# Optimization experiments

Hardware: AMD Instinct MI355X
Metric: run time of the kernel (lower is better)

The kernel has to match this reference:

```python
import jax, jax.numpy as jnp
import numpy as np

THETA = 10000.0


def apply_rope(t):
    """Partial rotary on first head_dim//2 dims, interleaved pairs (rotary_embedding_torch).
    t: (B, H, S, D) float32."""
    B, H, S, D = t.shape
    rot_dim = D // 2  # RotaryEmbedding(head_dim // 2)
    inv_freq = 1.0 / (THETA ** (jnp.arange(0, rot_dim, 2, dtype=jnp.float32) / rot_dim))  # (rot_dim//2,)
    pos = jnp.arange(S, dtype=jnp.float32)
    freqs = pos[:, None] * inv_freq[None, :]            # (S, rot_dim//2)
    freqs = jnp.repeat(freqs, 2, axis=-1)               # (S, rot_dim) interleaved
    cos, sin = jnp.cos(freqs), jnp.sin(freqs)           # (S, rot_dim)
    t_rot, t_pass = t[..., :rot_dim], t[..., rot_dim:]
    x1 = t_rot[..., 0::2]
    x2 = t_rot[..., 1::2]
    rot_half = jnp.stack((-x2, x1), axis=-1).reshape(t_rot.shape)
    t_rot = t_rot * cos + rot_half * sin
    return jnp.concatenate([t_rot, t_pass], axis=-1)


def setup_inputs() -> dict:
    key = jax.random.key(0)
    k1, k2, k3, k4, k5 = jax.random.split(key, 5)
    B, S, Dm = 2, 2048, 1024
    scale = 1.0 / np.sqrt(Dm)
    return {
        "x": jax.random.normal(k1, (B, S, Dm), dtype=jnp.float32),
        "Wqkv": jax.random.normal(k2, (3 * Dm, Dm), dtype=jnp.float32) * scale,
        "bqkv": jax.random.normal(k3, (3 * Dm,), dtype=jnp.float32) * 0.01,
        "Wout": jax.random.normal(k4, (Dm, Dm), dtype=jnp.float32) * scale,
        "bout": jax.random.normal(k5, (Dm,), dtype=jnp.float32) * 0.01,
    }


def reference(x, Wqkv, bqkv, Wout, bout):
    B, S, Dm = x.shape
    H = 16
    Dh = Dm // H
    qkv = x @ Wqkv.T + bqkv                              # (B, S, 3*Dm)
    qkv = qkv.reshape(B, S, 3, H, Dh).transpose(2, 0, 3, 1, 4)  # (3, B, H, S, Dh)
    q, k, v = qkv[0], qkv[1], qkv[2]
    q = apply_rope(q.astype(jnp.float32))
    k = apply_rope(k.astype(jnp.float32))
    scores = jnp.einsum("bhqd,bhkd->bhqk", q, k) / jnp.sqrt(jnp.float32(Dh))
    attn = jax.nn.softmax(scores, axis=-1)
    out = jnp.einsum("bhqk,bhkd->bhqd", attn, v)         # (B, H, S, Dh)
    out = out.transpose(0, 2, 1, 3).reshape(B, S, Dm)
    return out @ Wout.T + bout
```

## Files before the change

kernel.cpp:

```cpp
#include <hip/hip_runtime.h>

#define S_LEN 2048
#define DMODEL 1024
#define NHEAD 16
#define DHEAD 64
#define BATCH 2
#define BH_TOT (BATCH * NHEAD)
#define TOK (BATCH * S_LEN)
#define NQKV (3 * DMODEL)

#define QSCALE 0.18033688011112042f

typedef float  f32x4  __attribute__((ext_vector_type(4)));
typedef float  f32x16 __attribute__((ext_vector_type(16)));
typedef int    i32x4  __attribute__((ext_vector_type(4)));
typedef unsigned u32x2 __attribute__((ext_vector_type(2)));
typedef __bf16 bf16x8 __attribute__((ext_vector_type(8)));
typedef __bf16 bf16x4 __attribute__((ext_vector_type(4)));
typedef __bf16 bf16x2 __attribute__((ext_vector_type(2)));

typedef __attribute__((address_space(1))) void* as1_ptr;
typedef __attribute__((address_space(3))) void* as3_ptr;

__device__ __forceinline__ void gl2lds16(const void* g, void* l) {
  __builtin_amdgcn_global_load_lds((as1_ptr)(void*)g, (as3_ptr)l, 16, 0, 0);
}

__device__ __forceinline__ f32x4 mfma32(bf16x8 a, bf16x8 b, f32x4 c) {
  return __builtin_amdgcn_mfma_f32_16x16x32_bf16(a, b, c, 0, 0, 0);
}

__device__ __forceinline__ f32x16 mfma3216(bf16x8 a, bf16x8 b, f32x16 c) {
  return __builtin_amdgcn_mfma_f32_32x32x16_bf16(a, b, c, 0, 0, 0);
}

__device__ __forceinline__ unsigned pack2(float a, float b) {
  bf16x2 t;
  t[0] = (__bf16)a;
  t[1] = (__bf16)b;
  return __builtin_bit_cast(unsigned, t);
}

__device__ __forceinline__ bf16x8 pfragn(float a0, float a1, float a2, float a3,
                                         float a4, float a5, float a6, float a7) {
  const i32x4 w = {(int)pack2(a0, a1), (int)pack2(a2, a3),
                   (int)pack2(a4, a5), (int)pack2(a6, a7)};
  return __builtin_bit_cast(bf16x8, w);
}

__global__ __launch_bounds__(256) void cvt_kernel(const float* __restrict__ src,
                                                  __bf16* __restrict__ dst, int n) {
  const int i = (blockIdx.x * 256 + threadIdx.x) * 4;
  if (i >= n) return;
  const f32x4 v = *(const f32x4*)(src + i);
  bf16x4 o;
  o[0] = (__bf16)v[0]; o[1] = (__bf16)v[1]; o[2] = (__bf16)v[2]; o[3] = (__bf16)v[3];
  *(bf16x4*)(dst + i) = o;
}

__device__ __forceinline__ void gemm_tile_128(const __bf16* __restrict__ A,
                                              const __bf16* __restrict__ Bw,
                                              const int Kd, const int tileM, const int tileN,
                                              __bf16* As, __bf16* Bs, f32x4 acc[4][4]) {
  const int t    = threadIdx.x;
  const int lane = t & 63;
  const int wave = t >> 6;
  const int quad = lane >> 4;
  const int c    = lane & 15;
  const int wm   = (wave >> 1) << 6;
  const int wn   = (wave & 1) << 6;

  const int u0 = t, u1 = t + 256;
  const __bf16* gA0 = A  + (size_t)(tileM + (u0 >> 2)) * Kd + (u0 & 3) * 8;
  const __bf16* gA1 = A  + (size_t)(tileM + (u1 >> 2)) * Kd + (u1 & 3) * 8;
  const __bf16* gB0 = Bw + (size_t)(tileN + (u0 >> 2)) * Kd + (u0 & 3) * 8;
  const __bf16* gB1 = Bw + (size_t)(tileN + (u1 >> 2)) * Kd + (u1 & 3) * 8;
  __bf16* lA0 = As + u0 * 8; __bf16* lA1 = As + u1 * 8;
  __bf16* lB0 = Bs + u0 * 8; __bf16* lB1 = Bs + u1 * 8;

  for (int k0 = 0; k0 < Kd; k0 += 32) {
    gl2lds16(gA0 + k0, lA0);
    gl2lds16(gA1 + k0, lA1);
    gl2lds16(gB0 + k0, lB0);
    gl2lds16(gB1 + k0, lB1);
    __syncthreads();
    bf16x8 af[4], bfr[4];
#pragma unroll
    for (int mt = 0; mt < 4; ++mt)
      af[mt] = *(const bf16x8*)(As + (wm + mt * 16 + c) * 32 + quad * 8);
#pragma unroll
    for (int nt = 0; nt < 4; ++nt)
      bfr[nt] = *(const bf16x8*)(Bs + (wn + nt * 16 + c) * 32 + quad * 8);
#pragma unroll
    for (int mt = 0; mt < 4; ++mt)
#pragma unroll
      for (int nt = 0; nt < 4; ++nt)
        acc[mt][nt] = mfma32(af[mt], bfr[nt], acc[mt][nt]);
    __syncthreads();
  }
}

__global__ __launch_bounds__(256) void gemm_qkv_kernel(const __bf16* __restrict__ xb,
                                                       const __bf16* __restrict__ Wb,
                                                       const float* __restrict__ bias,
                                                       __bf16* __restrict__ Qb,
                                                       __bf16* __restrict__ Kb,
                                                       __bf16* __restrict__ Vtb) {
  __shared__ __align__(16) __bf16 As[128 * 32];
  __shared__ __align__(16) __bf16 Bs[128 * 32];
  f32x4 acc[4][4];
#pragma unroll
  for (int i = 0; i < 4; ++i)
#pragma unroll
    for (int j = 0; j < 4; ++j) acc[i][j] = (f32x4){0.f, 0.f, 0.f, 0.f};

  const int tileM = blockIdx.y * 128;
  const int tileN = blockIdx.x * 128;
  gemm_tile_128(xb, Wb, DMODEL, tileM, tileN, As, Bs, acc);

  const int t = threadIdx.x;
  const int lane = t & 63, wave = t >> 6;
  const int quad = lane >> 4, c = lane & 15;
  const int wm = (wave >> 1) << 6, wn = (wave & 1) << 6;

#pragma unroll
  for (int nt = 0; nt < 4; ++nt) {
    const int col = tileN + wn + nt * 16 + c;
    const float bv = bias[col];
    const int which = col >> 10;
    const int h  = (col >> 6) & 15;
    const int dh = col & 63;
    if (which == 2) {
#pragma unroll
      for (int mt = 0; mt < 4; ++mt) {
        const int row0 = tileM + wm + mt * 16 + quad * 4;
        const int bb = row0 >> 11;
        const int ss = row0 & (S_LEN - 1);
        bf16x4 o;
#pragma unroll
        for (int r = 0; r < 4; ++r) o[r] = (__bf16)(acc[mt][nt][r] + bv);
        *(bf16x4*)(Vtb + (((size_t)(bb * NHEAD + h)) * DHEAD + dh) * S_LEN + ss) = o;
      }
    } else {
      __bf16* dst = (which == 0) ? Qb : Kb;
      const float scl = (which == 0) ? QSCALE : 1.0f;
#pragma unroll
      for (int mt = 0; mt < 4; ++mt) {
#pragma unroll
        for (int r = 0; r < 4; ++r) {
          const int row = tileM + wm + mt * 16 + quad * 4 + r;
          const int bb = row >> 11;
          const int ss = row & (S_LEN - 1);
          dst[(((size_t)(bb * NHEAD + h)) * S_LEN + ss) * DHEAD + dh] =
              (__bf16)((acc[mt][nt][r] + bv) * scl);
        }
      }
    }
  }
}

__global__ __launch_bounds__(256) void gemm_out_kernel(const __bf16* __restrict__ AOb,
                                                       const __bf16* __restrict__ Wb,
                                                       const float* __restrict__ bout,
                                                       float* __restrict__ out) {
  __shared__ __align__(16) __bf16 As[128 * 32];
  __shared__ __align__(16) __bf16 Bs[128 * 32];
  f32x4 acc[4][4];
#pragma unroll
  for (int i = 0; i < 4; ++i)
#pragma unroll
    for (int j = 0; j < 4; ++j) acc[i][j] = (f32x4){0.f, 0.f, 0.f, 0.f};

  const int tileM = blockIdx.y * 128;
  const int tileN = blockIdx.x * 128;
  gemm_tile_128(AOb, Wb, DMODEL, tileM, tileN, As, Bs, acc);

  const int t = threadIdx.x;
  const int lane = t & 63, wave = t >> 6;
  const int quad = lane >> 4, c = lane & 15;
  const int wm = (wave >> 1) << 6, wn = (wave & 1) << 6;

#pragma unroll
  for (int nt = 0; nt < 4; ++nt) {
    const int col = tileN + wn + nt * 16 + c;
    const float bv = bout[col];
#pragma unroll
    for (int mt = 0; mt < 4; ++mt) {
#pragma unroll
      for (int r = 0; r < 4; ++r) {
        const int row = tileM + wm + mt * 16 + quad * 4 + r;
        out[(size_t)row * DMODEL + col] = acc[mt][nt][r] + bv;
      }
    }
  }
}

__global__ __launch_bounds__(256) void rope_kernel(__bf16* __restrict__ Qb, __bf16* __restrict__ Kb) {
  const int idx = blockIdx.x * 256 + threadIdx.x;
  const int j  = idx & 15;
  const int s  = (idx >> 4) & (S_LEN - 1);
  const int bh = (idx >> 15) & (BH_TOT - 1);
  __bf16* base = (idx >> 20) ? Kb : Qb;
  bf16x2* p = (bf16x2*)(base + ((size_t)bh * S_LEN + s) * DHEAD) + j;
  bf16x2 v = *p;
  const float x1 = (float)v[0];
  const float x2 = (float)v[1];
  const float LOG2_10000 = 13.287712379549449f;
  const float inv = exp2f(-(float)j * (LOG2_10000 / 16.0f));
  const float ang = (float)s * inv;
  float sn, cs;
  sincosf(ang, &sn, &cs);
  bf16x2 o;
  o[0] = (__bf16)(x1 * cs - x2 * sn);
  o[1] = (__bf16)(x2 * cs + x1 * sn);
  *p = o;
}

__global__ __launch_bounds__(64, 2) void attn_kernel(const __bf16* __restrict__ Qb,
                                                     const __bf16* __restrict__ Kb,
                                                     const __bf16* __restrict__ Vtb,
                                                     __bf16* __restrict__ AOb) {
  __shared__ __align__(16) __bf16 Ks[2][32 * 64];
  __shared__ __align__(16) __bf16 Vts[2][64 * 32];

  const int qt = blockIdx.x;
  const int bh = blockIdx.y;
  const int b = bh >> 4, h = bh & 15;
  const int lane = threadIdx.x & 63;
  const int c31 = lane & 31, hi = lane >> 5;
  const int cx7 = c31 & 7;
  const int cxv = (c31 >> 1) & 3;
  const size_t head = (size_t)bh * S_LEN * DHEAD;
  const int q0w = qt * 32;

  bf16x8 qf[4];
#pragma unroll
  for (int s = 0; s < 4; ++s)
    qf[s] = *(const bf16x8*)(Qb + head + (size_t)(q0w + c31) * DHEAD + s * 16 + hi * 8);

  f32x16 zzero;
#pragma unroll
  for (int i = 0; i < 16; ++i) zzero[i] = 0.f;

  f32x16 ota[2], otb[2];
  ota[0] = zzero; ota[1] = zzero; otb[0] = zzero; otb[1] = zzero;
  float lp = 0.f;

  const __bf16* kg[4];
  const __bf16* vg[4];
  int lofK[4], lofV[4];
#pragma unroll
  for (int i = 0; i < 4; ++i) {
    const int u = lane + 64 * i;
    const int rk = u >> 3, ck = (u & 7) ^ (rk & 7);
    kg[i] = Kb + head + (size_t)rk * DHEAD + ck * 8;
    lofK[i] = u * 8;
    const int rv = u >> 2, cv = (u & 3) ^ ((rv >> 1) & 3);
    vg[i] = Vtb + ((size_t)bh * DHEAD + rv) * S_LEN + cv * 8;
    lofV[i] = u * 8;
  }

#pragma unroll
  for (int i = 0; i < 4; ++i) {
    gl2lds16(kg[i], &Ks[0][lofK[i]]);
    gl2lds16(vg[i], &Vts[0][lofV[i]]);
  }

#define VFRAG(CUR, db, kc)                                                                 \
  __builtin_bit_cast(bf16x8, (i32x4){                                                      \
      (int)__builtin_bit_cast(u32x2, *(const bf16x4*)(&Vts[CUR][((db) * 32 + c31) * 32 +   \
                                     ((((kc) * 2) ^ cxv) * 8) + hi * 4]))[0],              \
      (int)__builtin_bit_cast(u32x2, *(const bf16x4*)(&Vts[CUR][((db) * 32 + c31) * 32 +   \
                                     ((((kc) * 2) ^ cxv) * 8) + hi * 4]))[1],              \
      (int)__builtin_bit_cast(u32x2, *(const bf16x4*)(&Vts[CUR][((db) * 32 + c31) * 32 +   \
                                     ((((kc) * 2 + 1) ^ cxv) * 8) + hi * 4]))[0],          \
      (int)__builtin_bit_cast(u32x2, *(const bf16x4*)(&Vts[CUR][((db) * 32 + c31) * 32 +   \
                                     ((((kc) * 2 + 1) ^ cxv) * 8) + hi * 4]))[1]})

#define ATTN_TILE(KB, CUR)                                                                 \
  {                                                                                        \
    asm volatile("s_waitcnt vmcnt(0)" ::: "memory");                                       \
    __builtin_amdgcn_sched_barrier(0);                                                     \
    bf16x8 kA[4];                                                                          \
    _Pragma("unroll")                                                                      \
    for (int s = 0; s < 4; ++s)                                                            \
      kA[s] = *(const bf16x8*)(&Ks[CUR][c31 * 64 + (((s * 2 + hi) ^ cx7) * 8)]);           \
    const bf16x8 vA00 = VFRAG(CUR, 0, 0);                                                  \
    const bf16x8 vA10 = VFRAG(CUR, 1, 0);                                                  \
    const bf16x8 vA01 = VFRAG(CUR, 0, 1);                                                  \
    const bf16x8 vA11 = VFRAG(CUR, 1, 1);                                                  \
    __builtin_amdgcn_sched_barrier(0);                                                     \
    if ((KB) + 1 < S_LEN / 32) {                                                           \
      const int ka = ((KB) + 1) * (32 * DHEAD);                                            \
      const int va = ((KB) + 1) * 32;                                                      \
      _Pragma("unroll")                                                                    \
      for (int i = 0; i < 4; ++i) {                                                        \
        gl2lds16(kg[i] + ka, &Ks[(CUR) ^ 1][lofK[i]]);                                     \
        gl2lds16(vg[i] + va, &Vts[(CUR) ^ 1][lofV[i]]);                                    \
      }                                                                                    \
    }                                                                                      \
    __builtin_amdgcn_sched_barrier(0);                                                     \
    f32x16 z = zzero;                                                                      \
    __builtin_amdgcn_s_setprio(1);                                                         \
    _Pragma("unroll")                                                                      \
    for (int s = 0; s < 4; ++s) z = mfma3216(kA[s], qf[s], z);                             \
    __builtin_amdgcn_s_setprio(0);                                                         \
    float p[16];                                                                           \
    _Pragma("unroll")                                                                      \
    for (int r = 0; r < 16; ++r) p[r] = __builtin_amdgcn_exp2f(z[r]);                      \
    lp += (((p[0] + p[1]) + (p[2] + p[3])) + ((p[4] + p[5]) + (p[6] + p[7])))              \
        + (((p[8] + p[9]) + (p[10] + p[11])) + ((p[12] + p[13]) + (p[14] + p[15])));       \
    const bf16x8 f0 = pfragn(p[0], p[1], p[2], p[3], p[4], p[5], p[6], p[7]);              \
    const bf16x8 f1 = pfragn(p[8], p[9], p[10], p[11], p[12], p[13], p[14], p[15]);        \
    __builtin_amdgcn_s_setprio(1);                                                         \
    ota[0] = mfma3216(vA00, f0, ota[0]);                                                   \
    ota[1] = mfma3216(vA10, f0, ota[1]);                                                   \
    otb[0] = mfma3216(vA01, f1, otb[0]);                                                   \
    otb[1] = mfma3216(vA11, f1, otb[1]);                                                   \
    __builtin_amdgcn_s_setprio(0);                                                         \
  }

  for (int kbb = 0; kbb < S_LEN / 64; ++kbb) {
    ATTN_TILE(2 * kbb, 0)
    ATTN_TILE(2 * kbb + 1, 1)
  }
#undef ATTN_TILE
#undef VFRAG

#pragma unroll
  for (int i = 0; i < 16; ++i) { ota[0][i] += otb[0][i]; ota[1][i] += otb[1][i]; }
  const float l = lp + __shfl_xor(lp, 32);
  const float inv = 1.0f / l;
  const int q = q0w + c31;
#pragma unroll
  for (int db = 0; db < 2; ++db) {
#pragma unroll
    for (int rg = 0; rg < 4; ++rg) {
      bf16x4 o;
#pragma unroll
      for (int i = 0; i < 4; ++i) o[i] = (__bf16)(ota[db][rg * 4 + i] * inv);
      const int d0 = db * 32 + rg * 8 + hi * 4;
      *(bf16x4*)(AOb + ((size_t)(b * S_LEN + q)) * DMODEL + h * DHEAD + d0) = o;
    }
  }
}

extern "C" void kernel_launch(void* const* d_in, const int* in_sizes, int n_in,
                              void* d_out, int out_size, void* d_ws, size_t ws_size,
                              hipStream_t stream) {
  const float* x    = (const float*)d_in[0];
  const float* Wqkv = (const float*)d_in[1];
  const float* bqkv = (const float*)d_in[2];
  const float* Wout = (const float*)d_in[3];
  const float* bout = (const float*)d_in[4];
  float* out = (float*)d_out;

  char* ws = (char*)d_ws;
  __bf16* xb    = (__bf16*)(ws + 0);
  __bf16* Wqkvb = (__bf16*)(ws + (size_t)8  * 1024 * 1024);
  __bf16* Woutb = (__bf16*)(ws + (size_t)14 * 1024 * 1024);
  __bf16* Qb    = (__bf16*)(ws + (size_t)16 * 1024 * 1024);
  __bf16* Kb    = (__bf16*)(ws + (size_t)24 * 1024 * 1024);
  __bf16* Vtb   = (__bf16*)(ws + (size_t)32 * 1024 * 1024);
  __bf16* AOb   = (__bf16*)(ws + (size_t)40 * 1024 * 1024);

  cvt_kernel<<<(TOK * DMODEL) / 1024, 256, 0, stream>>>(x, xb, TOK * DMODEL);
  cvt_kernel<<<(NQKV * DMODEL) / 1024, 256, 0, stream>>>(Wqkv, Wqkvb, NQKV * DMODEL);
  cvt_kernel<<<(DMODEL * DMODEL) / 1024, 256, 0, stream>>>(Wout, Woutb, DMODEL * DMODEL);

  gemm_qkv_kernel<<<dim3(NQKV / 128, TOK / 128), 256, 0, stream>>>(xb, Wqkvb, bqkv, Qb, Kb, Vtb);

  rope_kernel<<<(2 * BH_TOT * S_LEN * 16) / 256, 256, 0, stream>>>(Qb, Kb);

  attn_kernel<<<dim3(S_LEN / 32, BH_TOT), 64, 0, stream>>>(Qb, Kb, Vtb, AOb);

  gemm_out_kernel<<<dim3(DMODEL / 128, TOK / 128), 256, 0, stream>>>(AOb, Woutb, bout, out);
}
```

Baseline: 212.0 us.

## Share K/V tiles across two waves with 4-stage LDS prefetch pipeline

The attention kernel now runs two waves per block, each handling 32 query rows, so every K/V tile loaded into LDS serves 64 queries and global K/V traffic per query is halved. The LDS buffering grows from double to quad buffers with three tiles prefetched ahead, and waits use partial vmcnt counts instead of draining all loads. This adds a block barrier per tile and doubles LDS use per block, which may lower occupancy.

```diff
diff --git a/kernel.cpp b/kernel.cpp
--- a/kernel.cpp
+++ b/kernel.cpp
@@ -216,22 +216,23 @@
   *p = o;
 }
 
-__global__ __launch_bounds__(64, 2) void attn_kernel(const __bf16* __restrict__ Qb,
-                                                     const __bf16* __restrict__ Kb,
-                                                     const __bf16* __restrict__ Vtb,
-                                                     __bf16* __restrict__ AOb) {
-  __shared__ __align__(16) __bf16 Ks[2][32 * 64];
-  __shared__ __align__(16) __bf16 Vts[2][64 * 32];
+__global__ __launch_bounds__(128, 2) void attn_kernel(const __bf16* __restrict__ Qb,
+                                                      const __bf16* __restrict__ Kb,
+                                                      const __bf16* __restrict__ Vtb,
+                                                      __bf16* __restrict__ AOb) {
+  __shared__ __align__(16) __bf16 Ks[4][32 * 64];
+  __shared__ __align__(16) __bf16 Vts[4][64 * 32];
 
   const int qt = blockIdx.x;
   const int bh = blockIdx.y;
   const int b = bh >> 4, h = bh & 15;
-  const int lane = threadIdx.x & 63;
+  const int t = threadIdx.x;
+  const int wave = t >> 6, lane = t & 63;
   const int c31 = lane & 31, hi = lane >> 5;
   const int cx7 = c31 & 7;
   const int cxv = (c31 >> 1) & 3;
   const size_t head = (size_t)bh * S_LEN * DHEAD;
-  const int q0w = qt * 32;
+  const int q0w = qt * 64 + wave * 32;
 
   bf16x8 qf[4];
 #pragma unroll
@@ -246,12 +247,12 @@
   ota[0] = zzero; ota[1] = zzero; otb[0] = zzero; otb[1] = zzero;
   float lp = 0.f;
 
-  const __bf16* kg[4];
-  const __bf16* vg[4];
-  int lofK[4], lofV[4];
-#pragma unroll
-  for (int i = 0; i < 4; ++i) {
-    const int u = lane + 64 * i;
+  const __bf16* kg[2];
+  const __bf16* vg[2];
+  int lofK[2], lofV[2];
+#pragma unroll
+  for (int i = 0; i < 2; ++i) {
+    const int u = t + 128 * i;
     const int rk = u >> 3, ck = (u & 7) ^ (rk & 7);
     kg[i] = Kb + head + (size_t)rk * DHEAD + ck * 8;
     lofK[i] = u * 8;
@@ -261,9 +262,14 @@
   }
 
 #pragma unroll
-  for (int i = 0; i < 4; ++i) {
-    gl2lds16(kg[i], &Ks[0][lofK[i]]);
-    gl2lds16(vg[i], &Vts[0][lofV[i]]);
+  for (int tt = 0; tt < 3; ++tt) {
+    const int ka = tt * (32 * DHEAD);
+    const int va = tt * 32;
+#pragma unroll
+    for (int i = 0; i < 2; ++i) {
+      gl2lds16(kg[i] + ka, &Ks[tt][lofK[i]]);
+      gl2lds16(vg[i] + va, &Vts[tt][lofV[i]]);
+    }
   }
 
 #define VFRAG(CUR, db, kc)                                                                 \
@@ -277,9 +283,20 @@
       (int)__builtin_bit_cast(u32x2, *(const bf16x4*)(&Vts[CUR][((db) * 32 + c31) * 32 +   \
                                      ((((kc) * 2 + 1) ^ cxv) * 8) + hi * 4]))[1]})
 
-#define ATTN_TILE(KB, CUR)                                                                 \
+#define ATTN_TILE(KB, CUR, VM, PF)                                                         \
   {                                                                                        \
-    asm volatile("s_waitcnt vmcnt(0)" ::: "memory");                                       \
+    asm volatile("s_waitcnt vmcnt(" #VM ")" ::: "memory");                                 \
+    __builtin_amdgcn_s_barrier();                                                          \
+    __builtin_amdgcn_sched_barrier(0);                                                     \
+    if (PF) {                                                                              \
+      const int ka = ((KB) + 3) * (32 * DHEAD);                                            \
+      const int va = ((KB) + 3) * 32;                                                      \
+      _Pragma("unroll")                                                                    \
+      for (int i = 0; i < 2; ++i) {                                                        \
+        gl2lds16(kg[i] + ka, &Ks[((CUR) + 3) & 3][lofK[i]]);                               \
+        gl2lds16(vg[i] + va, &Vts[((CUR) + 3) & 3][lofV[i]]);                              \
+      }                                                                                    \
+    }                                                                                      \
     __builtin_amdgcn_sched_barrier(0);                                                     \
     bf16x8 kA[4];                                                                          \
     _Pragma("unroll")                                                                      \
@@ -289,17 +306,6 @@
     const bf16x8 vA10 = VFRAG(CUR, 1, 0);                                                  \
     const bf16x8 vA01 = VFRAG(CUR, 0, 1);                                                  \
     const bf16x8 vA11 = VFRAG(CUR, 1, 1);                                                  \
-    __builtin_amdgcn_sched_barrier(0);                                                     \
-    if ((KB) + 1 < S_LEN / 32) {                                                           \
-      const int ka = ((KB) + 1) * (32 * DHEAD);                                            \
-      const int va = ((KB) + 1) * 32;                                                      \
-      _Pragma("unroll")                                                                    \
-      for (int i = 0; i < 4; ++i) {                                                        \
-        gl2lds16(kg[i] + ka, &Ks[(CUR) ^ 1][lofK[i]]);                                     \
-        gl2lds16(vg[i] + va, &Vts[(CUR) ^ 1][lofV[i]]);                                    \
-      }                                                                                    \
-    }                                                                                      \
-    __builtin_amdgcn_sched_barrier(0);                                                     \
     f32x16 z = zzero;                                                                      \
     __builtin_amdgcn_s_setprio(1);                                                         \
     _Pragma("unroll")                                                                      \
@@ -320,10 +326,17 @@
     __builtin_amdgcn_s_setprio(0);                                                         \
   }
 
-  for (int kbb = 0; kbb < S_LEN / 64; ++kbb) {
-    ATTN_TILE(2 * kbb, 0)
-    ATTN_TILE(2 * kbb + 1, 1)
-  }
+  for (int kbb = 0; kbb < 15; ++kbb) {
+    const int kb4 = kbb * 4;
+    ATTN_TILE(kb4 + 0, 0, 8, 1)
+    ATTN_TILE(kb4 + 1, 1, 8, 1)
+    ATTN_TILE(kb4 + 2, 2, 8, 1)
+    ATTN_TILE(kb4 + 3, 3, 8, 1)
+  }
+  ATTN_TILE(60, 0, 8, 1)
+  ATTN_TILE(61, 1, 8, 0)
+  ATTN_TILE(62, 2, 4, 0)
+  ATTN_TILE(63, 3, 0, 0)
 #undef ATTN_TILE
 #undef VFRAG
 
@@ -372,7 +385,7 @@
 
   rope_kernel<<<(2 * BH_TOT * S_LEN * 16) / 256, 256, 0, stream>>>(Qb, Kb);
 
-  attn_kernel<<<dim3(S_LEN / 32, BH_TOT), 64, 0, stream>>>(Qb, Kb, Vtb, AOb);
+  attn_kernel<<<dim3(S_LEN / 64, BH_TOT), 128, 0, stream>>>(Qb, Kb, Vtb, AOb);
 
   gemm_out_kernel<<<dim3(DMODEL / 128, TOK / 128), 256, 0, stream>>>(AOb, Woutb, bout, out);
 }
```

After: 211.6 us. About the same (-0.2%).
